# Kernel tuning notes

Hardware: AMD Instinct MI355X
Metric: run time of the kernel (lower is better)

## Reference

```python
import jax, jax.numpy as jnp
import numpy as np

B, N = 16, 512          # graphs, nodes per graph (equal-size dynamic batch)
IN, HID, OUT, K = 256, 128, 256, 16  # hidden = in_dim // red_factor
EPS = 1e-5


def setup_inputs() -> dict:
    key = jax.random.key(0)
    ks = jax.random.split(key, 12)
    def lin(k, fi, fo):
        return jax.random.normal(k, (fi, fo), jnp.float32) / np.sqrt(fi).astype(np.float32)
    return {
        "obj_encs": jax.random.normal(ks[0], (B * N, IN), jnp.float32),
        "n_nodes": jnp.full((B,), N, dtype=jnp.int32),
        # self-graph-attention params (in -> hidden), with residual projection
        "Wq": lin(ks[1], IN, HID), "bq": jnp.zeros((HID,), jnp.float32),
        "Wk": lin(ks[2], IN, HID), "bk": jnp.zeros((HID,), jnp.float32),
        "Wv": lin(ks[3], IN, HID), "bv": jnp.zeros((HID,), jnp.float32),
        "Wr": lin(ks[4], IN, HID), "br": jnp.zeros((HID,), jnp.float32),
        # EdgeConv (local+global => 2*HID input features)
        "Wc": lin(ks[5], 2 * HID, OUT), "bc": jnp.zeros((OUT,), jnp.float32),
        # LayerNorm affine
        "ln_scale": jnp.ones((OUT,), jnp.float32),
        "ln_bias": jnp.zeros((OUT,), jnp.float32),
    }


def _forward(obj_encs, n_nodes, Wq, bq, Wk, bk, Wv, bv, Wr, br, Wc, bc, ln_scale, ln_bias):
    # dynamic batching: equal-size graphs per n_nodes -> reshape [B, N, IN]
    x = obj_encs.reshape(B, N, IN)

    # --- SelfGraphAttentionLinear (per-graph dot-product attention, residual) ---
    q = x @ Wq + bq                      # [B, N, HID]
    kk = x @ Wk + bk
    v = x @ Wv + bv
    attn = jax.nn.softmax(jnp.einsum('bnd,bmd->bnm', q, kk) / np.sqrt(HID).astype(np.float32), axis=-1)
    h = jnp.einsum('bnm,bmd->bnd', attn, v) + (x @ Wr + br)  # residual projection

    # --- GraphConv: kNN (euclidean) within each graph ---
    sq = jnp.sum(h * h, axis=-1)                             # [B, N]
    dist = sq[:, :, None] + sq[:, None, :] - 2.0 * jnp.einsum('bnd,bmd->bnm', h, h)
    _, idx = jax.lax.top_k(-dist, K)                         # [B, N, K] (self included)

    nb = jax.vmap(lambda hb, ib: hb[ib])(h, idx)             # [B, N, K, HID]
    hc = h[:, :, None, :]                                    # [B, N, 1, HID]
    # features='local+global': [x_i, x_j - x_i]
    e = jnp.concatenate([jnp.broadcast_to(hc, nb.shape), nb - hc], axis=-1)  # [B,N,K,2H]

    y = jnp.einsum('bnkf,fo->bnko', e, Wc) + bc              # [B, N, K, OUT]
    y = jnp.max(y, axis=2)                                   # reduction='max' over k

    mu = jnp.mean(y, axis=-1, keepdims=True)
    var = jnp.mean((y - mu) ** 2, axis=-1, keepdims=True)
    y = (y - mu) / jnp.sqrt(var + EPS) * ln_scale + ln_bias  # LayerNorm
    return jax.nn.selu(y).reshape(B * N, OUT)


def reference(obj_encs, n_nodes, Wq, bq, Wk, bk, Wv, bv, Wr, br, Wc, bc, ln_scale, ln_bias):
    return _forward(obj_encs, n_nodes, Wq, bq, Wk, bk, Wv, bv, Wr, br, Wc, bc, ln_scale, ln_bias)
```

## Files before the change

kernel.cpp:

```cpp
#include <hip/hip_runtime.h>
#include <math.h>

#define NB   16
#define NN   512
#define FIN  256
#define HID  128
#define FOUT 256
#define TOPK 16
#define ROWS (NB*NN)
#define LN_EPS 1e-5f

#define BK  32
#define LDK 40

typedef __attribute__((ext_vector_type(8)))  short  bf16x8;
typedef __attribute__((ext_vector_type(4)))  float  f32x4;
typedef __attribute__((ext_vector_type(8)))  unsigned short u16x8;

__device__ __forceinline__ ushort f2bf_rn(float x) {
    uint u = __float_as_uint(x);
    u += 0x7fff + ((u >> 16) & 1);
    return (ushort)(u >> 16);
}
__device__ __forceinline__ float bf2f(ushort h) {
    return __uint_as_float(((uint)h) << 16);
}
__device__ __forceinline__ void split2(float x, ushort& hi, ushort& lo) {
    hi = f2bf_rn(x);
    lo = f2bf_rn(x - bf2f(hi));
}

__device__ __forceinline__ void stage_u(ushort (*Ds)[LDK], const ushort* __restrict__ src,
                                        int rstride, int tid)
{
    const int r = tid >> 2, seg = (tid & 3) * 8;
    *(u16x8*)&Ds[r][seg] = *(const u16x8*)(src + (size_t)r * rstride + seg);
}

__device__ __forceinline__ void mma_step64(const ushort (*Ah)[LDK], const ushort (*Al)[LDK],
                                           const ushort (*Bh)[LDK], const ushort (*Bl)[LDK],
                                           f32x4 acc[2][2], int wr, int wc, int lane)
{
    const int q8 = (lane >> 4) * 8, m = lane & 15;
    bf16x8 ah[2], al[2], bh[2], bl[2];
    #pragma unroll
    for (int i = 0; i < 2; i++) {
        ah[i] = *(const bf16x8*)&Ah[wr + 16*i + m][q8];
        al[i] = *(const bf16x8*)&Al[wr + 16*i + m][q8];
        bh[i] = *(const bf16x8*)&Bh[wc + 16*i + m][q8];
        bl[i] = *(const bf16x8*)&Bl[wc + 16*i + m][q8];
    }
    #pragma unroll
    for (int i = 0; i < 2; i++)
        #pragma unroll
        for (int j = 0; j < 2; j++) {
            acc[i][j] = __builtin_amdgcn_mfma_f32_16x16x32_bf16(ah[i], bh[j], acc[i][j], 0, 0, 0);
            acc[i][j] = __builtin_amdgcn_mfma_f32_16x16x32_bf16(ah[i], bl[j], acc[i][j], 0, 0, 0);
            acc[i][j] = __builtin_amdgcn_mfma_f32_16x16x32_bf16(al[i], bh[j], acc[i][j], 0, 0, 0);
        }
}

#define MM64_PROLOGUE()                                                     \
    __shared__ ushort smem[4*64*LDK];                                       \
    ushort (*Ah)[LDK] = (ushort (*)[LDK])(smem);                            \
    ushort (*Al)[LDK] = (ushort (*)[LDK])(smem + 64*LDK);                   \
    ushort (*Bh)[LDK] = (ushort (*)[LDK])(smem + 2*64*LDK);                 \
    ushort (*Bl)[LDK] = (ushort (*)[LDK])(smem + 3*64*LDK);                 \
    float* fbuf = (float*)smem;   \
    const int tid = threadIdx.x, lane = tid & 63, wv = tid >> 6;            \
    const int wr = (wv >> 1) * 32, wc = (wv & 1) * 32;                      \
    f32x4 acc[2][2];                                                        \
    _Pragma("unroll")                                                       \
    for (int i = 0; i < 2; i++)                                             \
        _Pragma("unroll")                                                   \
        for (int j = 0; j < 2; j++)                                         \
            acc[i][j] = (f32x4){0.f, 0.f, 0.f, 0.f};

__global__ __launch_bounds__(256) void k_prep_w(
    const float* __restrict__ Wq, const float* __restrict__ Wk,
    const float* __restrict__ Wv, const float* __restrict__ Wr,
    const float* __restrict__ Wc,
    const float* __restrict__ bq, const float* __restrict__ bk,
    const float* __restrict__ bv, const float* __restrict__ br,
    const float* __restrict__ bc,
    ushort* __restrict__ Wth, ushort* __restrict__ Wtl,
    ushort* __restrict__ Wcth, ushort* __restrict__ Wctl,
    float* __restrict__ bcat, float* __restrict__ bcab,
    float* __restrict__ SQ)
{
    const int blk = blockIdx.x, tid = threadIdx.x;
    __shared__ float fb[64][65];

    if (blk < 8) {
        const int n0 = blk * 64;
        const int widx = n0 >> 7;
        const float* W = widx==0 ? Wq : widx==1 ? Wk : widx==2 ? Wv : Wr;
        const int cbase = n0 & 127;
        for (int kt = 0; kt < 4; kt++) {
            const int k0 = kt * 64;
            __syncthreads();
            {
                const int kk = tid >> 2, cs = (tid & 3) * 16;
                #pragma unroll
                for (int t = 0; t < 16; t += 4) {
                    const float4 q = *(const float4*)&W[(size_t)(k0+kk)*HID + cbase + cs + t];
                    fb[kk][cs+t]=q.x; fb[kk][cs+t+1]=q.y; fb[kk][cs+t+2]=q.z; fb[kk][cs+t+3]=q.w;
                }
            }
            __syncthreads();
            {
                const int c = tid >> 2, ks = (tid & 3) * 16;
                u16x8 vh0, vh1, vl0, vl1;
                #pragma unroll
                for (int t = 0; t < 8; t++) {
                    ushort hh, ll;
                    split2(fb[ks+t][c], hh, ll); vh0[t]=hh; vl0[t]=ll;
                    split2(fb[ks+8+t][c], hh, ll); vh1[t]=hh; vl1[t]=ll;
                }
                *(u16x8*)&Wth[(size_t)(n0+c)*256 + k0 + ks]     = vh0;
                *(u16x8*)&Wth[(size_t)(n0+c)*256 + k0 + ks + 8] = vh1;
                *(u16x8*)&Wtl[(size_t)(n0+c)*256 + k0 + ks]     = vl0;
                *(u16x8*)&Wtl[(size_t)(n0+c)*256 + k0 + ks + 8] = vl1;
            }
        }
    } else if (blk < 16) {
        const int n0 = (blk - 8) * 64;
        const bool ahalf = n0 < 256;
        const int cbase = n0 & 255;
        for (int kt = 0; kt < 2; kt++) {
            const int k0 = kt * 64;
            __syncthreads();
            {
                const int kk = tid >> 2, cs = (tid & 3) * 16;
                #pragma unroll
                for (int t = 0; t < 16; t++) {
                    const float bot = Wc[(size_t)(HID + k0 + kk)*FOUT + cbase + cs + t];
                    float val = bot;
                    if (ahalf) val = Wc[(size_t)(k0 + kk)*FOUT + cbase + cs + t] - bot;
                    fb[kk][cs+t] = val;
                }
            }
            __syncthreads();
            {
                const int c = tid >> 2, ks = (tid & 3) * 16;
                u16x8 vh0, vh1, vl0, vl1;
                #pragma unroll
                for (int t = 0; t < 8; t++) {
                    ushort hh, ll;
                    split2(fb[ks+t][c], hh, ll); vh0[t]=hh; vl0[t]=ll;
                    split2(fb[ks+8+t][c], hh, ll); vh1[t]=hh; vl1[t]=ll;
                }
                *(u16x8*)&Wcth[(size_t)(n0+c)*128 + k0 + ks]     = vh0;
                *(u16x8*)&Wcth[(size_t)(n0+c)*128 + k0 + ks + 8] = vh1;
                *(u16x8*)&Wctl[(size_t)(n0+c)*128 + k0 + ks]     = vl0;
                *(u16x8*)&Wctl[(size_t)(n0+c)*128 + k0 + ks + 8] = vl1;
            }
        }
    } else {
        for (int i = tid; i < 512; i += 256) {
            const int w = i >> 7, c = i & 127;
            bcat[i] = w==0 ? bq[c] : w==1 ? bk[c] : w==2 ? bv[c] : br[c];
            bcab[i] = i < 256 ? bc[i] : 0.f;
        }
        for (int i = tid; i < ROWS; i += 256) SQ[i] = 0.f;
    }
}

__global__ __launch_bounds__(256) void k_prep_x(
    const float* __restrict__ X, ushort* __restrict__ Xh, ushort* __restrict__ Xl)
{
    const size_t base = ((size_t)blockIdx.x * 256 + threadIdx.x) * 8;
    const float4 a = *(const float4*)(X + base);
    const float4 b = *(const float4*)(X + base + 4);
    u16x8 vh, vl; ushort hh, ll;
    split2(a.x,hh,ll); vh[0]=hh; vl[0]=ll;
    split2(a.y,hh,ll); vh[1]=hh; vl[1]=ll;
    split2(a.z,hh,ll); vh[2]=hh; vl[2]=ll;
    split2(a.w,hh,ll); vh[3]=hh; vl[3]=ll;
    split2(b.x,hh,ll); vh[4]=hh; vl[4]=ll;
    split2(b.y,hh,ll); vh[5]=hh; vl[5]=ll;
    split2(b.z,hh,ll); vh[6]=hh; vl[6]=ll;
    split2(b.w,hh,ll); vh[7]=hh; vl[7]=ll;
    *(u16x8*)(Xh + base) = vh;
    *(u16x8*)(Xl + base) = vl;
}

__global__ __launch_bounds__(256) void k_proj_m(
    const ushort* __restrict__ Xh, const ushort* __restrict__ Xl,
    const ushort* __restrict__ Wth, const ushort* __restrict__ Wtl,
    const float* __restrict__ bcat,
    ushort* __restrict__ Yh, ushort* __restrict__ Yl,
    ushort* __restrict__ Vth, ushort* __restrict__ Vtl,
    float* __restrict__ Rbuf)
{
    const int ct  = blockIdx.x;
    const int br0 = blockIdx.y * 64;

    MM64_PROLOGUE();

    for (int k0 = 0; k0 < FIN; k0 += BK) {
        stage_u(Ah, Xh + (size_t)br0 * 256 + k0, 256, tid);
        stage_u(Al, Xl + (size_t)br0 * 256 + k0, 256, tid);
        stage_u(Bh, Wth + (size_t)(ct*64) * 256 + k0, 256, tid);
        stage_u(Bl, Wtl + (size_t)(ct*64) * 256 + k0, 256, tid);
        __syncthreads();
        mma_step64(Ah, Al, Bh, Bl, acc, wr, wc, lane);
        __syncthreads();
    }

    {
        const int m = lane & 15, q4 = (lane >> 4) * 4;
        #pragma unroll
        for (int i = 0; i < 2; i++)
            #pragma unroll
            for (int reg = 0; reg < 4; reg++) {
                const int r = wr + 16*i + q4 + reg;
                #pragma unroll
                for (int j = 0; j < 2; j++) {
                    const int c = wc + 16*j + m;
                    fbuf[r*65 + c] = acc[i][j][reg] + bcat[ct*64 + c];
                }
            }
    }
    __syncthreads();

    if (ct < 4) {
        const int r = tid >> 2, cs = (tid & 3) * 16;
        u16x8 vh0, vh1, vl0, vl1;
        #pragma unroll
        for (int t = 0; t < 8; t++) {
            ushort hh, ll;
            split2(fbuf[r*65 + cs + t], hh, ll);     vh0[t]=hh; vl0[t]=ll;
            split2(fbuf[r*65 + cs + 8 + t], hh, ll); vh1[t]=hh; vl1[t]=ll;
        }
        const size_t o = (size_t)(br0 + r) * 256 + ct*64 + cs;
        *(u16x8*)&Yh[o]   = vh0; *(u16x8*)&Yh[o+8] = vh1;
        *(u16x8*)&Yl[o]   = vl0; *(u16x8*)&Yl[o+8] = vl1;
    } else if (ct < 6) {
        const int cl = tid >> 2, rs = (tid & 3) * 16;
        const int b = br0 >> 9, nb = br0 & 511;
        const int cglob = (ct - 4) * 64 + cl;
        u16x8 vh0, vh1, vl0, vl1;
        #pragma unroll
        for (int t = 0; t < 8; t++) {
            ushort hh, ll;
            split2(fbuf[(rs+t)*65 + cl], hh, ll);   vh0[t]=hh; vl0[t]=ll;
            split2(fbuf[(rs+8+t)*65 + cl], hh, ll); vh1[t]=hh; vl1[t]=ll;
        }
        const size_t o = ((size_t)b*128 + cglob) * 512 + nb + rs;
        *(u16x8*)&Vth[o]   = vh0; *(u16x8*)&Vth[o+8] = vh1;
        *(u16x8*)&Vtl[o]   = vl0; *(u16x8*)&Vtl[o+8] = vl1;
    } else {
        const int r = tid >> 2, cs = (tid & 3) * 16;
        float* dst = Rbuf + (size_t)(br0 + r) * 128 + (ct - 6)*64 + cs;
        #pragma unroll
        for (int t = 0; t < 16; t += 4) {
            float4 q;
            q.x = fbuf[r*65+cs+t];   q.y = fbuf[r*65+cs+t+1];
            q.z = fbuf[r*65+cs+t+2]; q.w = fbuf[r*65+cs+t+3];
            *(float4*)(dst + t) = q;
        }
    }
}

__global__ __launch_bounds__(256) void k_scores_m(
    const ushort* __restrict__ Yh, const ushort* __restrict__ Yl,
    float* __restrict__ S)
{
    const int b = blockIdx.z;
    const int m0 = blockIdx.x * 64, n0 = blockIdx.y * 64;
    const float scale = 0.08838834764831845f;

    MM64_PROLOGUE();

    for (int k0 = 0; k0 < HID; k0 += BK) {
        stage_u(Ah, Yh + (size_t)(b*NN + n0) * 256 + k0,       256, tid);
        stage_u(Al, Yl + (size_t)(b*NN + n0) * 256 + k0,       256, tid);
        stage_u(Bh, Yh + (size_t)(b*NN + m0) * 256 + 128 + k0, 256, tid);
        stage_u(Bl, Yl + (size_t)(b*NN + m0) * 256 + 128 + k0, 256, tid);
        __syncthreads();
        mma_step64(Ah, Al, Bh, Bl, acc, wr, wc, lane);
        __syncthreads();
    }

    float* Sb = S + (size_t)b * NN * NN;
    const int m = lane & 15, q4 = (lane >> 4) * 4;
    #pragma unroll
    for (int i = 0; i < 2; i++)
        #pragma unroll
        for (int reg = 0; reg < 4; reg++) {
            const int n = n0 + wr + 16*i + q4 + reg;
            #pragma unroll
            for (int j = 0; j < 2; j++)
                Sb[(size_t)n * NN + m0 + wc + 16*j + m] = acc[i][j][reg] * scale;
        }
}

__global__ __launch_bounds__(256) void k_softmax2(
    const float* __restrict__ S, ushort* __restrict__ Ph, ushort* __restrict__ Pl)
{
    const size_t row = blockIdx.x;
    const float* p = S + row * NN;
    const int tid = threadIdx.x, lane = tid & 63, wave = tid >> 6;
    __shared__ float red[4];

    const float2 vv = ((const float2*)p)[tid];
    float mx = fmaxf(vv.x, vv.y);
    #pragma unroll
    for (int off = 32; off > 0; off >>= 1) mx = fmaxf(mx, __shfl_down(mx, off));
    if (lane == 0) red[wave] = mx;
    __syncthreads();
    mx = fmaxf(fmaxf(red[0], red[1]), fmaxf(red[2], red[3]));
    __syncthreads();

    const float e0 = __expf(vv.x - mx), e1 = __expf(vv.y - mx);
    float s = e0 + e1;
    #pragma unroll
    for (int off = 32; off > 0; off >>= 1) s += __shfl_down(s, off);
    if (lane == 0) red[wave] = s;
    __syncthreads();
    s = red[0] + red[1] + red[2] + red[3];
    const float inv = 1.0f / s;

    ushort h0,l0,h1,l1;
    split2(e0 * inv, h0, l0);
    split2(e1 * inv, h1, l1);
    ((ushort2*)Ph)[row * 256 + tid] = make_ushort2(h0, h1);
    ((ushort2*)Pl)[row * 256 + tid] = make_ushort2(l0, l1);
}

__global__ __launch_bounds__(256) void k_hgemm_m(
    const ushort* __restrict__ Ph, const ushort* __restrict__ Pl,
    const ushort* __restrict__ Vth, const ushort* __restrict__ Vtl,
    const float* __restrict__ Rbuf,
    ushort* __restrict__ Hh, ushort* __restrict__ Hl,
    float* __restrict__ SQ)
{
    const int c0 = blockIdx.x * 64;
    const int n0 = blockIdx.y * 64;
    const int b  = blockIdx.z;

    MM64_PROLOGUE();

    for (int k0 = 0; k0 < NN; k0 += BK) {
        stage_u(Ah, Ph + (size_t)(b*NN + n0) * 512 + k0, 512, tid);
        stage_u(Al, Pl + (size_t)(b*NN + n0) * 512 + k0, 512, tid);
        stage_u(Bh, Vth + ((size_t)b*128 + c0) * 512 + k0, 512, tid);
        stage_u(Bl, Vtl + ((size_t)b*128 + c0) * 512 + k0, 512, tid);
        __syncthreads();
        mma_step64(Ah, Al, Bh, Bl, acc, wr, wc, lane);
        __syncthreads();
    }

    {
        const int m = lane & 15, q4 = (lane >> 4) * 4;
        #pragma unroll
        for (int i = 0; i < 2; i++)
            #pragma unroll
            for (int reg = 0; reg < 4; reg++) {
                const int r = wr + 16*i + q4 + reg;
                #pragma unroll
                for (int j = 0; j < 2; j++)
                    fbuf[r*65 + wc + 16*j + m] = acc[i][j][reg];
            }
    }
    __syncthreads();

    {
        const int r = tid >> 2, cs = (tid & 3) * 16;
        const int gr = b*NN + n0 + r;
        const float* rp = Rbuf + (size_t)gr * 128 + c0 + cs;
        float h[16]; float sqp = 0.f;
        #pragma unroll
        for (int t = 0; t < 16; t += 4) {
            const float4 q = *(const float4*)(rp + t);
            h[t]   = fbuf[r*65+cs+t]   + q.x;
            h[t+1] = fbuf[r*65+cs+t+1] + q.y;
            h[t+2] = fbuf[r*65+cs+t+2] + q.z;
            h[t+3] = fbuf[r*65+cs+t+3] + q.w;
        }
        u16x8 vh0, vh1, vl0, vl1;
        #pragma unroll
        for (int t = 0; t < 8; t++) {
            ushort hh, ll;
            split2(h[t], hh, ll);   vh0[t]=hh; vl0[t]=ll;
            split2(h[8+t], hh, ll); vh1[t]=hh; vl1[t]=ll;
            sqp += h[t]*h[t] + h[8+t]*h[8+t];
        }
        const size_t o = (size_t)gr * 128 + c0 + cs;
        *(u16x8*)&Hh[o]   = vh0; *(u16x8*)&Hh[o+8] = vh1;
        *(u16x8*)&Hl[o]   = vl0; *(u16x8*)&Hl[o+8] = vl1;
        sqp += __shfl_xor(sqp, 1);
        sqp += __shfl_xor(sqp, 2);
        if ((tid & 3) == 0) atomicAdd(&SQ[gr], sqp);
    }
}

__global__ __launch_bounds__(256) void k_ab_m(
    const ushort* __restrict__ Hh, const ushort* __restrict__ Hl,
    const ushort* __restrict__ Wcth, const ushort* __restrict__ Wctl,
    const float* __restrict__ bcab, float* __restrict__ AB)
{
    const int ct  = blockIdx.x;
    const int br0 = blockIdx.y * 64;

    MM64_PROLOGUE();

    for (int k0 = 0; k0 < HID; k0 += BK) {
        stage_u(Ah, Hh + (size_t)br0 * 128 + k0, 128, tid);
        stage_u(Al, Hl + (size_t)br0 * 128 + k0, 128, tid);
        stage_u(Bh, Wcth + (size_t)(ct*64) * 128 + k0, 128, tid);
        stage_u(Bl, Wctl + (size_t)(ct*64) * 128 + k0, 128, tid);
        __syncthreads();
        mma_step64(Ah, Al, Bh, Bl, acc, wr, wc, lane);
        __syncthreads();
    }

    const int m = lane & 15, q4 = (lane >> 4) * 4;
    #pragma unroll
    for (int i = 0; i < 2; i++)
        #pragma unroll
        for (int reg = 0; reg < 4; reg++) {
            const int grow = br0 + wr + 16*i + q4 + reg;
            #pragma unroll
            for (int j = 0; j < 2; j++) {
                const int c = wc + 16*j + m;
                AB[(size_t)grow * 512 + ct*64 + c] = acc[i][j][reg] + bcab[ct*64 + c];
            }
        }
}

__global__ __launch_bounds__(256) void k_dist_m(
    const ushort* __restrict__ Hh, const ushort* __restrict__ Hl,
    const float* __restrict__ SQ, float* __restrict__ D)
{
    const int b = blockIdx.z;
    const int m0 = blockIdx.x * 64, n0 = blockIdx.y * 64;

    MM64_PROLOGUE();

    for (int k0 = 0; k0 < HID; k0 += BK) {
        stage_u(Ah, Hh + (size_t)(b*NN + n0) * 128 + k0, 128, tid);
        stage_u(Al, Hl + (size_t)(b*NN + n0) * 128 + k0, 128, tid);
        stage_u(Bh, Hh + (size_t)(b*NN + m0) * 128 + k0, 128, tid);
        stage_u(Bl, Hl + (size_t)(b*NN + m0) * 128 + k0, 128, tid);
        __syncthreads();
        mma_step64(Ah, Al, Bh, Bl, acc, wr, wc, lane);
        __syncthreads();
    }

    const int gb = b * NN;
    float* Db = D + (size_t)b * NN * NN;
    const int m = lane & 15, q4 = (lane >> 4) * 4;
    float sqm[2];
    #pragma unroll
    for (int j = 0; j < 2; j++) sqm[j] = SQ[gb + m0 + wc + 16*j + m];
    #pragma unroll
    for (int i = 0; i < 2; i++)
        #pragma unroll
        for (int reg = 0; reg < 4; reg++) {
            const int n = n0 + wr + 16*i + q4 + reg;
            const float sqn = SQ[gb + n];
            #pragma unroll
            for (int j = 0; j < 2; j++)
                Db[(size_t)n * NN + m0 + wc + 16*j + m]
                    = sqn + sqm[j] - 2.0f * acc[i][j][reg];
        }
}

__global__ __launch_bounds__(256) void k_out(
    const float* __restrict__ D, const float* __restrict__ AB,
    const float* __restrict__ ln_scale, const float* __restrict__ ln_bias,
    float* __restrict__ out)
{
    const int row  = blockIdx.x * 4 + (threadIdx.x >> 6);
    const int lane = threadIdx.x & 63;
    const int gb0  = row & ~(NN - 1);

    const float* drow = D + (size_t)row * NN;
    const float4 q0 = ((const float4*)drow)[lane];
    const float4 q1 = ((const float4*)drow)[64 + lane];
    float v[8] = {q0.x, q0.y, q0.z, q0.w, q1.x, q1.y, q1.z, q1.w};

    const float lsc0 = ln_scale[lane],       lbi0 = ln_bias[lane];
    const float lsc1 = ln_scale[lane + 64],  lbi1 = ln_bias[lane + 64];
    const float lsc2 = ln_scale[lane + 128], lbi2 = ln_bias[lane + 128];
    const float lsc3 = ln_scale[lane + 192], lbi3 = ln_bias[lane + 192];
    const float* arow = AB + (size_t)row * 512;
    const float a0 = arow[lane], a1 = arow[lane + 64],
                a2 = arow[lane + 128], a3 = arow[lane + 192];

    float bm0 = -INFINITY, bm1 = -INFINITY, bm2 = -INFINITY, bm3 = -INFINITY;

    for (int it = 0; it < TOPK; it++) {
        float bestv = v[0]; int bestm = 4*lane;
        #pragma unroll
        for (int j = 1; j < 8; j++) {
            const int m = (j >> 2)*256 + 4*lane + (j & 3);
            if (v[j] < bestv) { bestv = v[j]; bestm = m; }
        }
        #pragma unroll
        for (int off = 1; off < 64; off <<= 1) {
            const float ov = __shfl_xor(bestv, off);
            const int   om = __shfl_xor(bestm, off);
            if (ov < bestv || (ov == bestv && om < bestm)) { bestv = ov; bestm = om; }
        }
        const float* brow = AB + (size_t)(gb0 + bestm) * 512 + 256;
        bm0 = fmaxf(bm0, brow[lane]);
        bm1 = fmaxf(bm1, brow[lane + 64]);
        bm2 = fmaxf(bm2, brow[lane + 128]);
        bm3 = fmaxf(bm3, brow[lane + 192]);
        if (((bestm >> 2) & 63) == lane) {
            const int jj = ((bestm >> 8) << 2) | (bestm & 3);
            #pragma unroll
            for (int j = 0; j < 8; j++) if (j == jj) v[j] = INFINITY;
        }
    }

    float y0 = a0 + bm0, y1 = a1 + bm1, y2 = a2 + bm2, y3 = a3 + bm3;

    float s = y0 + y1 + y2 + y3;
    #pragma unroll
    for (int off = 1; off < 64; off <<= 1) s += __shfl_xor(s, off);
    const float mu = s * (1.0f/256.0f);
    const float d0 = y0 - mu, d1 = y1 - mu, d2 = y2 - mu, d3 = y3 - mu;
    float s2 = d0*d0 + d1*d1 + d2*d2 + d3*d3;
    #pragma unroll
    for (int off = 1; off < 64; off <<= 1) s2 += __shfl_xor(s2, off);
    const float var = s2 * (1.0f/256.0f);
    const float rstd = rsqrtf(var + LN_EPS);

    const float lam = 1.0507009873554805f, alpha = 1.6732632423543772f;
    float* orow = out + (size_t)row * FOUT;
    { const float z = d0*rstd*lsc0 + lbi0; orow[lane]       = z > 0.f ? lam*z : lam*alpha*expm1f(z); }
    { const float z = d1*rstd*lsc1 + lbi1; orow[lane + 64]  = z > 0.f ? lam*z : lam*alpha*expm1f(z); }
    { const float z = d2*rstd*lsc2 + lbi2; orow[lane + 128] = z > 0.f ? lam*z : lam*alpha*expm1f(z); }
    { const float z = d3*rstd*lsc3 + lbi3; orow[lane + 192] = z > 0.f ? lam*z : lam*alpha*expm1f(z); }
}

extern "C" void kernel_launch(void* const* d_in, const int* in_sizes, int n_in,
                              void* d_out, int out_size, void* d_ws, size_t ws_size,
                              hipStream_t stream)
{
    (void)in_sizes; (void)n_in; (void)out_size; (void)ws_size;
    const float* X   = (const float*)d_in[0];
    const float* Wq  = (const float*)d_in[2];
    const float* bq  = (const float*)d_in[3];
    const float* Wk  = (const float*)d_in[4];
    const float* bk  = (const float*)d_in[5];
    const float* Wv  = (const float*)d_in[6];
    const float* bv  = (const float*)d_in[7];
    const float* Wr  = (const float*)d_in[8];
    const float* br  = (const float*)d_in[9];
    const float* Wc  = (const float*)d_in[10];
    const float* bc  = (const float*)d_in[11];
    const float* lns = (const float*)d_in[12];
    const float* lnb = (const float*)d_in[13];
    float* out = (float*)d_out;

    char* cur = (char*)d_ws;
    auto alloc = [&](size_t bytes) { char* p = cur; cur += (bytes + 255) & ~size_t(255); return p; };

    float*  S    = (float*)alloc((size_t)NB*NN*NN*4);
    float*  AB   = (float*)alloc((size_t)ROWS*512*4);
    float*  Rbuf = (float*)alloc((size_t)ROWS*128*4);
    float*  SQ   = (float*)alloc((size_t)ROWS*4);
    float*  bcat = (float*)alloc(512*4);
    float*  bcab = (float*)alloc(512*4);
    ushort* Xh   = (ushort*)alloc((size_t)ROWS*256*2);
    ushort* Xl   = (ushort*)alloc((size_t)ROWS*256*2);
    ushort* Yh   = (ushort*)alloc((size_t)ROWS*256*2);
    ushort* Yl   = (ushort*)alloc((size_t)ROWS*256*2);
    ushort* Vth  = (ushort*)alloc((size_t)NB*128*512*2);
    ushort* Vtl  = (ushort*)alloc((size_t)NB*128*512*2);
    ushort* Ph   = (ushort*)alloc((size_t)ROWS*512*2);
    ushort* Pl   = (ushort*)alloc((size_t)ROWS*512*2);
    ushort* Hh   = (ushort*)alloc((size_t)ROWS*128*2);
    ushort* Hl   = (ushort*)alloc((size_t)ROWS*128*2);
    ushort* Wth  = (ushort*)alloc((size_t)512*256*2);
    ushort* Wtl  = (ushort*)alloc((size_t)512*256*2);
    ushort* Wcth = (ushort*)alloc((size_t)512*128*2);
    ushort* Wctl = (ushort*)alloc((size_t)512*128*2);
    float*  D    = S;

    k_prep_w  <<<17,           256, 0, stream>>>(Wq,Wk,Wv,Wr,Wc, bq,bk,bv,br,bc,
                                                 Wth,Wtl,Wcth,Wctl, bcat,bcab, SQ);
    k_prep_x  <<<ROWS*256/(256*8), 256, 0, stream>>>(X, Xh, Xl);
    k_proj_m  <<<dim3(8,128),  256, 0, stream>>>(Xh,Xl, Wth,Wtl, bcat, Yh,Yl, Vth,Vtl, Rbuf);
    k_scores_m<<<dim3(8,8,16), 256, 0, stream>>>(Yh,Yl, S);
    k_softmax2<<<ROWS,         256, 0, stream>>>(S, Ph, Pl);
    k_hgemm_m <<<dim3(2,8,16), 256, 0, stream>>>(Ph,Pl, Vth,Vtl, Rbuf, Hh,Hl, SQ);
    k_ab_m    <<<dim3(8,128),  256, 0, stream>>>(Hh,Hl, Wcth,Wctl, bcab, AB);
    k_dist_m  <<<dim3(8,8,16), 256, 0, stream>>>(Hh,Hl, SQ, D);
    k_out     <<<ROWS/4,       256, 0, stream>>>(D, AB, lns, lnb, out);
}
```

Baseline: 196.5 us.

## Fuse attention scores, softmax and PV into flash-style kernel; merge prep kernels

Replaces the separate score GEMM, softmax and P·V GEMM kernels with a single online-softmax attention kernel. Each wave holds 16 query rows in registers, streams keys and V^T straight from global memory, and keeps running max and sum statistics. This removes the round trips of the 16×512×512 score matrix and the split P matrices through HBM. It also folds the X split into the weight-prep kernel and writes SQ directly instead of zeroing it and using atomics. The tradeoff is only 256 blocks of 128 threads and no shared-memory staging of K/V, so K/V are reloaded from L2 per block and the GPU may be underfilled.

Result: slower. 232.9 us (+18.5%).

```diff
diff --git a/kernel.cpp b/kernel.cpp
--- a/kernel.cpp
+++ b/kernel.cpp
@@ -17,6 +17,11 @@
 typedef __attribute__((ext_vector_type(4)))  float  f32x4;
 typedef __attribute__((ext_vector_type(8)))  unsigned short u16x8;
 
+#define MFMA3(d, ah, al, bh, bl)                                              \
+    d = __builtin_amdgcn_mfma_f32_16x16x32_bf16(ah, bh, d, 0, 0, 0);          \
+    d = __builtin_amdgcn_mfma_f32_16x16x32_bf16(ah, bl, d, 0, 0, 0);          \
+    d = __builtin_amdgcn_mfma_f32_16x16x32_bf16(al, bh, d, 0, 0, 0);
+
 __device__ __forceinline__ ushort f2bf_rn(float x) {
     uint u = __float_as_uint(x);
     u += 0x7fff + ((u >> 16) & 1);
@@ -54,9 +59,7 @@
     for (int i = 0; i < 2; i++)
         #pragma unroll
         for (int j = 0; j < 2; j++) {
-            acc[i][j] = __builtin_amdgcn_mfma_f32_16x16x32_bf16(ah[i], bh[j], acc[i][j], 0, 0, 0);
-            acc[i][j] = __builtin_amdgcn_mfma_f32_16x16x32_bf16(ah[i], bl[j], acc[i][j], 0, 0, 0);
-            acc[i][j] = __builtin_amdgcn_mfma_f32_16x16x32_bf16(al[i], bh[j], acc[i][j], 0, 0, 0);
+            MFMA3(acc[i][j], ah[i], al[i], bh[j], bl[j]);
         }
 }
 
@@ -66,7 +69,7 @@
     ushort (*Al)[LDK] = (ushort (*)[LDK])(smem + 64*LDK);                   \
     ushort (*Bh)[LDK] = (ushort (*)[LDK])(smem + 2*64*LDK);                 \
     ushort (*Bl)[LDK] = (ushort (*)[LDK])(smem + 3*64*LDK);                 \
-    float* fbuf = (float*)smem;   \
+    float* fbuf = (float*)smem;                         \
     const int tid = threadIdx.x, lane = tid & 63, wv = tid >> 6;            \
     const int wr = (wv >> 1) * 32, wc = (wv & 1) * 32;                      \
     f32x4 acc[2][2];                                                        \
@@ -76,20 +79,39 @@
         for (int j = 0; j < 2; j++)                                         \
             acc[i][j] = (f32x4){0.f, 0.f, 0.f, 0.f};
 
-__global__ __launch_bounds__(256) void k_prep_w(
+__global__ __launch_bounds__(256) void k_prep(
     const float* __restrict__ Wq, const float* __restrict__ Wk,
     const float* __restrict__ Wv, const float* __restrict__ Wr,
     const float* __restrict__ Wc,
     const float* __restrict__ bq, const float* __restrict__ bk,
     const float* __restrict__ bv, const float* __restrict__ br,
     const float* __restrict__ bc,
+    const float* __restrict__ X,
     ushort* __restrict__ Wth, ushort* __restrict__ Wtl,
     ushort* __restrict__ Wcth, ushort* __restrict__ Wctl,
     float* __restrict__ bcat, float* __restrict__ bcab,
-    float* __restrict__ SQ)
+    ushort* __restrict__ Xh, ushort* __restrict__ Xl)
 {
     const int blk = blockIdx.x, tid = threadIdx.x;
     __shared__ float fb[64][65];
+
+    if (blk >= 17) {
+        const size_t base = ((size_t)(blk - 17) * 256 + tid) * 8;
+        const float4 a = *(const float4*)(X + base);
+        const float4 b = *(const float4*)(X + base + 4);
+        u16x8 vh, vl; ushort hh, ll;
+        split2(a.x,hh,ll); vh[0]=hh; vl[0]=ll;
+        split2(a.y,hh,ll); vh[1]=hh; vl[1]=ll;
+        split2(a.z,hh,ll); vh[2]=hh; vl[2]=ll;
+        split2(a.w,hh,ll); vh[3]=hh; vl[3]=ll;
+        split2(b.x,hh,ll); vh[4]=hh; vl[4]=ll;
+        split2(b.y,hh,ll); vh[5]=hh; vl[5]=ll;
+        split2(b.z,hh,ll); vh[6]=hh; vl[6]=ll;
+        split2(b.w,hh,ll); vh[7]=hh; vl[7]=ll;
+        *(u16x8*)(Xh + base) = vh;
+        *(u16x8*)(Xl + base) = vl;
+        return;
+    }
 
     if (blk < 8) {
         const int n0 = blk * 64;
@@ -162,27 +184,7 @@
             bcat[i] = w==0 ? bq[c] : w==1 ? bk[c] : w==2 ? bv[c] : br[c];
             bcab[i] = i < 256 ? bc[i] : 0.f;
         }
-        for (int i = tid; i < ROWS; i += 256) SQ[i] = 0.f;
-    }
-}
-
-__global__ __launch_bounds__(256) void k_prep_x(
-    const float* __restrict__ X, ushort* __restrict__ Xh, ushort* __restrict__ Xl)
-{
-    const size_t base = ((size_t)blockIdx.x * 256 + threadIdx.x) * 8;
-    const float4 a = *(const float4*)(X + base);
-    const float4 b = *(const float4*)(X + base + 4);
-    u16x8 vh, vl; ushort hh, ll;
-    split2(a.x,hh,ll); vh[0]=hh; vl[0]=ll;
-    split2(a.y,hh,ll); vh[1]=hh; vl[1]=ll;
-    split2(a.z,hh,ll); vh[2]=hh; vl[2]=ll;
-    split2(a.w,hh,ll); vh[3]=hh; vl[3]=ll;
-    split2(b.x,hh,ll); vh[4]=hh; vl[4]=ll;
-    split2(b.y,hh,ll); vh[5]=hh; vl[5]=ll;
-    split2(b.z,hh,ll); vh[6]=hh; vl[6]=ll;
-    split2(b.w,hh,ll); vh[7]=hh; vl[7]=ll;
-    *(u16x8*)(Xh + base) = vh;
-    *(u16x8*)(Xl + base) = vl;
+    }
 }
 
 __global__ __launch_bounds__(256) void k_proj_m(
@@ -263,136 +265,127 @@
     }
 }
 
-__global__ __launch_bounds__(256) void k_scores_m(
+__global__ __launch_bounds__(128) void k_attn(
     const ushort* __restrict__ Yh, const ushort* __restrict__ Yl,
-    float* __restrict__ S)
-{
-    const int b = blockIdx.z;
-    const int m0 = blockIdx.x * 64, n0 = blockIdx.y * 64;
-    const float scale = 0.08838834764831845f;
-
-    MM64_PROLOGUE();
-
-    for (int k0 = 0; k0 < HID; k0 += BK) {
-        stage_u(Ah, Yh + (size_t)(b*NN + n0) * 256 + k0,       256, tid);
-        stage_u(Al, Yl + (size_t)(b*NN + n0) * 256 + k0,       256, tid);
-        stage_u(Bh, Yh + (size_t)(b*NN + m0) * 256 + 128 + k0, 256, tid);
-        stage_u(Bl, Yl + (size_t)(b*NN + m0) * 256 + 128 + k0, 256, tid);
-        __syncthreads();
-        mma_step64(Ah, Al, Bh, Bl, acc, wr, wc, lane);
-        __syncthreads();
-    }
-
-    float* Sb = S + (size_t)b * NN * NN;
-    const int m = lane & 15, q4 = (lane >> 4) * 4;
-    #pragma unroll
-    for (int i = 0; i < 2; i++)
-        #pragma unroll
-        for (int reg = 0; reg < 4; reg++) {
-            const int n = n0 + wr + 16*i + q4 + reg;
-            #pragma unroll
-            for (int j = 0; j < 2; j++)
-                Sb[(size_t)n * NN + m0 + wc + 16*j + m] = acc[i][j][reg] * scale;
-        }
-}
-
-__global__ __launch_bounds__(256) void k_softmax2(
-    const float* __restrict__ S, ushort* __restrict__ Ph, ushort* __restrict__ Pl)
-{
-    const size_t row = blockIdx.x;
-    const float* p = S + row * NN;
-    const int tid = threadIdx.x, lane = tid & 63, wave = tid >> 6;
-    __shared__ float red[4];
-
-    const float2 vv = ((const float2*)p)[tid];
-    float mx = fmaxf(vv.x, vv.y);
-    #pragma unroll
-    for (int off = 32; off > 0; off >>= 1) mx = fmaxf(mx, __shfl_down(mx, off));
-    if (lane == 0) red[wave] = mx;
-    __syncthreads();
-    mx = fmaxf(fmaxf(red[0], red[1]), fmaxf(red[2], red[3]));
-    __syncthreads();
-
-    const float e0 = __expf(vv.x - mx), e1 = __expf(vv.y - mx);
-    float s = e0 + e1;
-    #pragma unroll
-    for (int off = 32; off > 0; off >>= 1) s += __shfl_down(s, off);
-    if (lane == 0) red[wave] = s;
-    __syncthreads();
-    s = red[0] + red[1] + red[2] + red[3];
-    const float inv = 1.0f / s;
-
-    ushort h0,l0,h1,l1;
-    split2(e0 * inv, h0, l0);
-    split2(e1 * inv, h1, l1);
-    ((ushort2*)Ph)[row * 256 + tid] = make_ushort2(h0, h1);
-    ((ushort2*)Pl)[row * 256 + tid] = make_ushort2(l0, l1);
-}
-
-__global__ __launch_bounds__(256) void k_hgemm_m(
-    const ushort* __restrict__ Ph, const ushort* __restrict__ Pl,
     const ushort* __restrict__ Vth, const ushort* __restrict__ Vtl,
     const float* __restrict__ Rbuf,
     ushort* __restrict__ Hh, ushort* __restrict__ Hl,
     float* __restrict__ SQ)
 {
-    const int c0 = blockIdx.x * 64;
-    const int n0 = blockIdx.y * 64;
-    const int b  = blockIdx.z;
-
-    MM64_PROLOGUE();
-
-    for (int k0 = 0; k0 < NN; k0 += BK) {
-        stage_u(Ah, Ph + (size_t)(b*NN + n0) * 512 + k0, 512, tid);
-        stage_u(Al, Pl + (size_t)(b*NN + n0) * 512 + k0, 512, tid);
-        stage_u(Bh, Vth + ((size_t)b*128 + c0) * 512 + k0, 512, tid);
-        stage_u(Bl, Vtl + ((size_t)b*128 + c0) * 512 + k0, 512, tid);
-        __syncthreads();
-        mma_step64(Ah, Al, Bh, Bl, acc, wr, wc, lane);
-        __syncthreads();
-    }
-
+    const int wv = threadIdx.x >> 6, lane = threadIdx.x & 63;
+    const int b  = blockIdx.x >> 4;
+    const int n0 = (blockIdx.x & 15) * 32 + wv * 16;
+    const int L = lane & 15, quad = lane >> 4;
+    const int grow0 = b * NN + n0;
+    const float scale = 0.08838834764831845f;
+
+    __shared__ ushort Pb[2][2][16][68];
+    ushort (*Pbh)[68] = Pb[wv][0];
+    ushort (*Pbl)[68] = Pb[wv][1];
+
+    bf16x8 qh[4], ql[4];
     {
-        const int m = lane & 15, q4 = (lane >> 4) * 4;
-        #pragma unroll
-        for (int i = 0; i < 2; i++)
-            #pragma unroll
-            for (int reg = 0; reg < 4; reg++) {
-                const int r = wr + 16*i + q4 + reg;
-                #pragma unroll
-                for (int j = 0; j < 2; j++)
-                    fbuf[r*65 + wc + 16*j + m] = acc[i][j][reg];
-            }
-    }
-    __syncthreads();
-
-    {
-        const int r = tid >> 2, cs = (tid & 3) * 16;
-        const int gr = b*NN + n0 + r;
-        const float* rp = Rbuf + (size_t)gr * 128 + c0 + cs;
-        float h[16]; float sqp = 0.f;
-        #pragma unroll
-        for (int t = 0; t < 16; t += 4) {
-            const float4 q = *(const float4*)(rp + t);
-            h[t]   = fbuf[r*65+cs+t]   + q.x;
-            h[t+1] = fbuf[r*65+cs+t+1] + q.y;
-            h[t+2] = fbuf[r*65+cs+t+2] + q.z;
-            h[t+3] = fbuf[r*65+cs+t+3] + q.w;
-        }
-        u16x8 vh0, vh1, vl0, vl1;
-        #pragma unroll
-        for (int t = 0; t < 8; t++) {
-            ushort hh, ll;
-            split2(h[t], hh, ll);   vh0[t]=hh; vl0[t]=ll;
-            split2(h[8+t], hh, ll); vh1[t]=hh; vl1[t]=ll;
-            sqp += h[t]*h[t] + h[8+t]*h[8+t];
-        }
-        const size_t o = (size_t)gr * 128 + c0 + cs;
-        *(u16x8*)&Hh[o]   = vh0; *(u16x8*)&Hh[o+8] = vh1;
-        *(u16x8*)&Hl[o]   = vl0; *(u16x8*)&Hl[o+8] = vl1;
-        sqp += __shfl_xor(sqp, 1);
-        sqp += __shfl_xor(sqp, 2);
-        if ((tid & 3) == 0) atomicAdd(&SQ[gr], sqp);
+        const ushort* q1 = Yh + (size_t)(grow0 + L) * 256 + quad * 8;
+        const ushort* q2 = Yl + (size_t)(grow0 + L) * 256 + quad * 8;
+        #pragma unroll
+        for (int s = 0; s < 4; s++) {
+            qh[s] = *(const bf16x8*)(q1 + 32*s);
+            ql[s] = *(const bf16x8*)(q2 + 32*s);
+        }
+    }
+
+    f32x4 O[8];
+    #pragma unroll
+    for (int j = 0; j < 8; j++) O[j] = (f32x4){0.f,0.f,0.f,0.f};
+    float m_i[4] = {-INFINITY,-INFINITY,-INFINITY,-INFINITY};
+    float l_i[4] = {0.f,0.f,0.f,0.f};
+
+    for (int m0 = 0; m0 < NN; m0 += 64) {
+        f32x4 Sf[4];
+        #pragma unroll
+        for (int j = 0; j < 4; j++) Sf[j] = (f32x4){0.f,0.f,0.f,0.f};
+        #pragma unroll
+        for (int s = 0; s < 4; s++) {
+            #pragma unroll
+            for (int j = 0; j < 4; j++) {
+                const size_t ko = (size_t)(b*NN + m0 + 16*j + L) * 256 + 128 + 32*s + quad*8;
+                bf16x8 kh = *(const bf16x8*)(Yh + ko);
+                bf16x8 kl = *(const bf16x8*)(Yl + ko);
+                MFMA3(Sf[j], qh[s], ql[s], kh, kl);
+            }
+        }
+        #pragma unroll
+        for (int j = 0; j < 4; j++)
+            #pragma unroll
+            for (int r = 0; r < 4; r++) Sf[j][r] *= scale;
+
+        float nm[4], al[4];
+        #pragma unroll
+        for (int r = 0; r < 4; r++) {
+            float mx = fmaxf(fmaxf(Sf[0][r], Sf[1][r]), fmaxf(Sf[2][r], Sf[3][r]));
+            mx = fmaxf(mx, __shfl_xor(mx, 1));
+            mx = fmaxf(mx, __shfl_xor(mx, 2));
+            mx = fmaxf(mx, __shfl_xor(mx, 4));
+            mx = fmaxf(mx, __shfl_xor(mx, 8));
+            nm[r] = fmaxf(m_i[r], mx);
+            al[r] = __expf(m_i[r] - nm[r]);
+            m_i[r] = nm[r];
+        }
+        float rs[4] = {0.f,0.f,0.f,0.f};
+        #pragma unroll
+        for (int j = 0; j < 4; j++) {
+            #pragma unroll
+            for (int r = 0; r < 4; r++) {
+                const float p = __expf(Sf[j][r] - nm[r]);
+                rs[r] += p;
+                ushort hh, ll; split2(p, hh, ll);
+                Pbh[quad*4 + r][16*j + L] = hh;
+                Pbl[quad*4 + r][16*j + L] = ll;
+            }
+        }
+        #pragma unroll
+        for (int r = 0; r < 4; r++) {
+            float s2 = rs[r];
+            s2 += __shfl_xor(s2, 1); s2 += __shfl_xor(s2, 2);
+            s2 += __shfl_xor(s2, 4); s2 += __shfl_xor(s2, 8);
+            l_i[r] = l_i[r] * al[r] + s2;
+        }
+        #pragma unroll
+        for (int j = 0; j < 8; j++)
+            #pragma unroll
+            for (int r = 0; r < 4; r++) O[j][r] *= al[r];
+
+        #pragma unroll
+        for (int s = 0; s < 2; s++) {
+            bf16x8 ph = *(const bf16x8*)&Pbh[L][32*s + quad*8];
+            bf16x8 pl = *(const bf16x8*)&Pbl[L][32*s + quad*8];
+            #pragma unroll
+            for (int j = 0; j < 8; j++) {
+                const size_t vo = ((size_t)(b*128 + 16*j + L)) * 512 + m0 + 32*s + quad*8;
+                bf16x8 vh = *(const bf16x8*)(Vth + vo);
+                bf16x8 vl = *(const bf16x8*)(Vtl + vo);
+                MFMA3(O[j], ph, pl, vh, vl);
+            }
+        }
+    }
+
+    #pragma unroll
+    for (int r = 0; r < 4; r++) {
+        const int grow = grow0 + quad*4 + r;
+        const float invl = 1.0f / l_i[r];
+        float sq = 0.f;
+        #pragma unroll
+        for (int j = 0; j < 8; j++) {
+            const int c = 16*j + L;
+            const float h = O[j][r] * invl + Rbuf[(size_t)grow*128 + c];
+            sq += h*h;
+            ushort hh, ll; split2(h, hh, ll);
+            Hh[(size_t)grow*128 + c] = hh;
+            Hl[(size_t)grow*128 + c] = ll;
+        }
+        sq += __shfl_xor(sq, 1); sq += __shfl_xor(sq, 2);
+        sq += __shfl_xor(sq, 4); sq += __shfl_xor(sq, 8);
+        if (L == 0) SQ[grow] = sq;
     }
 }
 
@@ -561,7 +554,7 @@
     char* cur = (char*)d_ws;
     auto alloc = [&](size_t bytes) { char* p = cur; cur += (bytes + 255) & ~size_t(255); return p; };
 
-    float*  S    = (float*)alloc((size_t)NB*NN*NN*4);
+    float*  Dst  = (float*)alloc((size_t)NB*NN*NN*4);
     float*  AB   = (float*)alloc((size_t)ROWS*512*4);
     float*  Rbuf = (float*)alloc((size_t)ROWS*128*4);
     float*  SQ   = (float*)alloc((size_t)ROWS*4);
@@ -573,24 +566,19 @@
     ushort* Yl   = (ushort*)alloc((size_t)ROWS*256*2);
     ushort* Vth  = (ushort*)alloc((size_t)NB*128*512*2);
     ushort* Vtl  = (ushort*)alloc((size_t)NB*128*512*2);
-    ushort* Ph   = (ushort*)alloc((size_t)ROWS*512*2);
-    ushort* Pl   = (ushort*)alloc((size_t)ROWS*512*2);
     ushort* Hh   = (ushort*)alloc((size_t)ROWS*128*2);
     ushort* Hl   = (ushort*)alloc((size_t)ROWS*128*2);
     ushort* Wth  = (ushort*)alloc((size_t)512*256*2);
     ushort* Wtl  = (ushort*)alloc((size_t)512*256*2);
     ushort* Wcth = (ushort*)alloc((size_t)512*128*2);
     ushort* Wctl = (ushort*)alloc((size_t)512*128*2);
-    float*  D    = S;
-
-    k_prep_w  <<<17,           256, 0, stream>>>(Wq,Wk,Wv,Wr,Wc, bq,bk,bv,br,bc,
-                                                 Wth,Wtl,Wcth,Wctl, bcat,bcab, SQ);
-    k_prep_x  <<<ROWS*256/(256*8), 256, 0, stream>>>(X, Xh, Xl);
-    k_proj_m  <<<dim3(8,128),  256, 0, stream>>>(Xh,Xl, Wth,Wtl, bcat, Yh,Yl, Vth,Vtl, Rbuf);
-    k_scores_m<<<dim3(8,8,16), 256, 0, stream>>>(Yh,Yl, S);
-    k_softmax2<<<ROWS,         256, 0, stream>>>(S, Ph, Pl);
-    k_hgemm_m <<<dim3(2,8,16), 256, 0, stream>>>(Ph,Pl, Vth,Vtl, Rbuf, Hh,Hl, SQ);
-    k_ab_m    <<<dim3(8,128),  256, 0, stream>>>(Hh,Hl, Wcth,Wctl, bcab, AB);
-    k_dist_m  <<<dim3(8,8,16), 256, 0, stream>>>(Hh,Hl, SQ, D);
-    k_out     <<<ROWS/4,       256, 0, stream>>>(D, AB, lns, lnb, out);
-}
+
+    k_prep   <<<17 + ROWS*256/(256*8), 256, 0, stream>>>(
+                 Wq,Wk,Wv,Wr,Wc, bq,bk,bv,br,bc, X,
+                 Wth,Wtl,Wcth,Wctl, bcat,bcab, Xh,Xl);
+    k_proj_m <<<dim3(8,128),  256, 0, stream>>>(Xh,Xl, Wth,Wtl, bcat, Yh,Yl, Vth,Vtl, Rbuf);
+    k_attn   <<<NB*16,        128, 0, stream>>>(Yh,Yl, Vth,Vtl, Rbuf, Hh,Hl, SQ);
+    k_ab_m   <<<dim3(8,128),  256, 0, stream>>>(Hh,Hl, Wcth,Wctl, bcab, AB);
+    k_dist_m <<<dim3(8,8,16), 256, 0, stream>>>(Hh,Hl, SQ, Dst);
+    k_out    <<<ROWS/4,       256, 0, stream>>>(Dst, AB, lns, lnb, out);
+}
```
